# Performance work log

Measured on AMD Instinct MI355X. Metric: run time of the kernel, lower is better.

## Reference

```python
import jax, jax.numpy as jnp
import numpy as np

# Functional model of IntegerLookup.call (CPU DenseHashTable path) applied to a
# fresh table containing only the pre-inserted OOV key (-1 -> 0), i.e. the
# first call after construction. Semantics of that call:
#   - flatten inputs, take unique keys in order of first occurrence
#   - assign contiguous ids starting at table.size()==1, up to max_tokens inserts
#   - keys beyond capacity (and anything not inserted) look up to default 0
# Note: the original code's `vals <= 0` test also re-inserts -1 itself, so -1
# is treated like any other key on the first call; we reproduce that exactly by
# not special-casing -1.

def _integer_lookup(inputs, max_tokens):
    shape = inputs.shape
    x = inputs.reshape(-1)
    n = x.shape[0]
    big = jnp.iinfo(x.dtype).max
    # unique keys (padded to fixed size n) + inverse map element -> unique slot
    uniq, inv = jnp.unique(x, return_inverse=True, size=n, fill_value=big)
    inv = inv.reshape(-1)
    # first-occurrence position of each unique key (padded slots keep sentinel n)
    first_idx = jnp.full((n,), n, dtype=jnp.int32).at[inv].min(
        jnp.arange(n, dtype=jnp.int32))
    # rank uniques by order of first appearance (padded slots sort last)
    rank = jnp.argsort(jnp.argsort(first_idx)).astype(jnp.int32)
    # table starts with size 1 (the -1 -> 0 OOV entry), so ids start at 1;
    # only the first `max_tokens` new keys fit (num_empty_slot), rest -> 0
    id_per_unique = jnp.where(rank < max_tokens, rank + 1, 0).astype(x.dtype)
    return id_per_unique[inv].reshape(shape)


def setup_inputs() -> dict:
    key = jax.random.key(0)
    inputs = jax.random.randint(key, (16384, 200), 0, 2000000, dtype=jnp.int32)
    return {"inputs": inputs, "max_tokens": 1000000}


def reference(inputs, max_tokens):
    return _integer_lookup(inputs, max_tokens)
```

## Files before the change

kernel.cpp:

```cpp
#include <hip/hip_runtime.h>
#include <stdint.h>

#define TABLE_BITS 21
#define TABLE_SIZE (1u << TABLE_BITS)
#define TABLE_MASK (TABLE_SIZE - 1u)
#define BLOCK 256
#define EPT 4
#define CHUNK (BLOCK * EPT)
#define EPT2 16
#define CHUNK2 (BLOCK * EPT2)
#define RANK_BIT 0x40000000
#define RANK_MASK 0x3FFFFFFF
#define NB 256
#define BSHIFT (TABLE_BITS - 8)
#define KPB (1 << BSHIFT)
#define KLOW_MASK (KPB - 1)
#define INF_PAT 0x7f7f7f7f
#define BJ_INVALID 0xFFFFFFFFu

template<int NT>
__device__ __forceinline__ int blk_excl_scan(int v, int tid, int* total) {
    constexpr int NW = NT / 64;
    int lane = tid & 63, w = tid >> 6;
    int inc = v;
    #pragma unroll
    for (int off = 1; off < 64; off <<= 1) {
        int u = __shfl_up(inc, off, 64);
        if (lane >= off) inc += u;
    }
    __shared__ int part[NW];
    if (lane == 63) part[w] = inc;
    __syncthreads();
    if (tid < NW) {
        int p = part[tid];
        #pragma unroll
        for (int off = 1; off < NW; off <<= 1) {
            int u = __shfl_up(p, off, 64);
            if (tid >= off) p += u;
        }
        part[tid] = p;
    }
    __syncthreads();
    int excl = ((w == 0) ? 0 : part[w - 1]) + inc - v;
    int tot = part[NW - 1];
    __syncthreads();
    if (total) *total = tot;
    return excl;
}

__global__ __launch_bounds__(BLOCK) void k_hist(const int* __restrict__ x, int n,
                                                unsigned* __restrict__ hist) {
    __shared__ unsigned cnt[NB];
    int tid = threadIdx.x;
    cnt[tid] = 0;
    __syncthreads();
    int e0 = blockIdx.x * CHUNK2;
    #pragma unroll
    for (int k = 0; k < EPT2 / 4; ++k) {
        int idx = e0 + k * (BLOCK * 4) + tid * 4;
        if (idx + 4 <= n) {
            int4 v = *reinterpret_cast<const int4*>(x + idx);
            atomicAdd(&cnt[((unsigned)v.x & TABLE_MASK) >> BSHIFT], 1u);
            atomicAdd(&cnt[((unsigned)v.y & TABLE_MASK) >> BSHIFT], 1u);
            atomicAdd(&cnt[((unsigned)v.z & TABLE_MASK) >> BSHIFT], 1u);
            atomicAdd(&cnt[((unsigned)v.w & TABLE_MASK) >> BSHIFT], 1u);
        } else {
            for (int i = idx; i < n; ++i)
                atomicAdd(&cnt[((unsigned)x[i] & TABLE_MASK) >> BSHIFT], 1u);
        }
    }
    __syncthreads();
    hist[(size_t)blockIdx.x * NB + tid] = cnt[tid];
}

__global__ __launch_bounds__(256) void k_colscan(unsigned* __restrict__ hist, int SB2,
                                                 unsigned* __restrict__ bucketTot) {
    int j = blockIdx.x, tid = threadIdx.x;
    unsigned carry = 0;
    for (int b0 = 0; b0 < SB2; b0 += 256) {
        int b = b0 + tid;
        int v = (b < SB2) ? (int)hist[(size_t)b * NB + j] : 0;
        int tot;
        int excl = blk_excl_scan<256>(v, tid, &tot);
        if (b < SB2) hist[(size_t)b * NB + j] = carry + (unsigned)excl;
        carry += (unsigned)tot;
    }
    if (tid == 0) bucketTot[j] = carry;
}

__global__ __launch_bounds__(256) void k_bucketbase(const unsigned* __restrict__ bucketTot,
                                                    unsigned* __restrict__ bucketBase) {
    int tid = threadIdx.x;
    int v = (int)bucketTot[tid];
    int tot;
    int excl = blk_excl_scan<256>(v, tid, &tot);
    bucketBase[tid] = (unsigned)excl;
    if (tid == 255) bucketBase[256] = (unsigned)(excl + v);
}

__global__ __launch_bounds__(BLOCK) void k_scatter(const int* __restrict__ x, int n,
                                                   const unsigned* __restrict__ hist,
                                                   const unsigned* __restrict__ bucketBase,
                                                   unsigned long long* __restrict__ pairs) {
    __shared__ unsigned cnt[NB];
    __shared__ unsigned lbase[NB + 1];
    __shared__ unsigned sbase[NB];
    __shared__ unsigned long long lp[CHUNK2];
    int tid = threadIdx.x;
    cnt[tid] = 0;
    sbase[tid] = bucketBase[tid] + hist[(size_t)blockIdx.x * NB + tid];
    __syncthreads();

    unsigned bjs[EPT2], kls[EPT2], los[EPT2];
    int e0 = blockIdx.x * CHUNK2;
    #pragma unroll
    for (int k = 0; k < EPT2 / 4; ++k) {
        int idx = e0 + k * (BLOCK * 4) + tid * 4;
        if (idx + 4 <= n) {
            int4 v = *reinterpret_cast<const int4*>(x + idx);
            unsigned kk[4] = {(unsigned)v.x & TABLE_MASK, (unsigned)v.y & TABLE_MASK,
                              (unsigned)v.z & TABLE_MASK, (unsigned)v.w & TABLE_MASK};
            #pragma unroll
            for (int j = 0; j < 4; ++j) {
                int e = k * 4 + j;
                bjs[e] = kk[j] >> BSHIFT;
                kls[e] = kk[j] & KLOW_MASK;
                los[e] = atomicAdd(&cnt[bjs[e]], 1u);
            }
        } else {
            #pragma unroll
            for (int j = 0; j < 4; ++j) {
                int e = k * 4 + j;
                int i = idx + j;
                if (i < n) {
                    unsigned kv = (unsigned)x[i] & TABLE_MASK;
                    bjs[e] = kv >> BSHIFT;
                    kls[e] = kv & KLOW_MASK;
                    los[e] = atomicAdd(&cnt[bjs[e]], 1u);
                } else {
                    bjs[e] = BJ_INVALID;
                }
            }
        }
    }
    __syncthreads();
    {
        int v = (int)cnt[tid];
        int tot;
        int ex = blk_excl_scan<256>(v, tid, &tot);
        lbase[tid] = (unsigned)ex;
        if (tid == 255) lbase[256] = (unsigned)(ex + v);
    }
    __syncthreads();
    #pragma unroll
    for (int k = 0; k < EPT2 / 4; ++k) {
        #pragma unroll
        for (int j = 0; j < 4; ++j) {
            int e = k * 4 + j;
            if (bjs[e] != BJ_INVALID) {
                unsigned pos = (unsigned)(e0 + k * (BLOCK * 4) + tid * 4 + j);
                lp[lbase[bjs[e]] + los[e]] =
                    ((unsigned long long)kls[e] << 32) | pos;
            }
        }
    }
    __syncthreads();
    int wv = tid >> 6, ln = tid & 63;
    for (int j = wv; j < NB; j += BLOCK / 64) {
        unsigned ls = lbase[j], len = lbase[j + 1] - ls, gs = sbase[j];
        for (unsigned i = ln; i < len; i += 64)
            pairs[gs + i] = lp[ls + i];
    }
}

__global__ __launch_bounds__(512) void k_bucket_min(const unsigned long long* __restrict__ pairs,
                                                    const unsigned* __restrict__ bucketBase,
                                                    int* __restrict__ table,
                                                    unsigned char* __restrict__ flag) {
    __shared__ int fi[KPB];
    int j = blockIdx.x, tid = threadIdx.x;
    for (int k = tid; k < KPB; k += 512) fi[k] = INF_PAT;
    __syncthreads();
    unsigned s = bucketBase[j], e = bucketBase[j + 1];
    for (unsigned idx = s + tid; idx < e; idx += 512) {
        unsigned long long p = pairs[idx];
        atomicMin(&fi[(unsigned)(p >> 32)], (int)(unsigned)p);
    }
    __syncthreads();
    int* dst = table + (size_t)j * KPB;
    for (int k = tid; k < KPB; k += 512) dst[k] = fi[k];
    for (unsigned idx = s + tid; idx < e; idx += 512) {
        unsigned long long p = pairs[idx];
        unsigned pos = (unsigned)p;
        flag[pos] = (unsigned char)(fi[(unsigned)(p >> 32)] == (int)pos);
    }
}

__global__ __launch_bounds__(BLOCK) void k_flags(const unsigned char* __restrict__ flag, int n,
                                                 int* __restrict__ blockSums,
                                                 unsigned long long* __restrict__ bitmask) {
    int tid = threadIdx.x;
    int lane = tid & 63, w = tid >> 6;
    int base = blockIdx.x * CHUNK + tid * EPT;
    int flags[EPT];
    if (base + EPT <= n) {
        uchar4 f = *reinterpret_cast<const uchar4*>(flag + base);
        flags[0] = f.x; flags[1] = f.y; flags[2] = f.z; flags[3] = f.w;
    } else {
        #pragma unroll
        for (int j = 0; j < EPT; ++j)
            flags[j] = (base + j < n) ? flag[base + j] : 0;
    }
    int cnt = 0;
    #pragma unroll
    for (int j = 0; j < EPT; ++j) {
        unsigned long long mj = __ballot(flags[j]);
        if (lane == 0) bitmask[((size_t)blockIdx.x * (BLOCK / 64) + w) * EPT + j] = mj;
        cnt += flags[j];
    }
    for (int off = 32; off > 0; off >>= 1)
        cnt += __shfl_down(cnt, off, 64);
    __shared__ int ws[BLOCK / 64];
    if (lane == 0) ws[w] = cnt;
    __syncthreads();
    if (tid == 0) {
        int s = 0;
        #pragma unroll
        for (int q = 0; q < BLOCK / 64; ++q) s += ws[q];
        blockSums[blockIdx.x] = s;
    }
}

__global__ __launch_bounds__(1024) void k_scan(int* __restrict__ sums, int B) {
    int tid = threadIdx.x;
    int carry = 0;
    for (int b0 = 0; b0 < B; b0 += 1024) {
        int b = b0 + tid;
        int v = (b < B) ? sums[b] : 0;
        int tot;
        int excl = blk_excl_scan<1024>(v, tid, &tot);
        if (b < B) sums[b] = carry + excl;
        carry += tot;
    }
}

__global__ __launch_bounds__(BLOCK) void k_rank(const int* __restrict__ x, int n,
                                                int* __restrict__ table,
                                                const int* __restrict__ blockSums,
                                                const unsigned long long* __restrict__ bitmask) {
    int tid = threadIdx.x;
    int lane = tid & 63, w = tid >> 6;
    int base = blockIdx.x * CHUNK + tid * EPT;
    const unsigned long long* bm = bitmask + ((size_t)blockIdx.x * (BLOCK / 64) + w) * EPT;
    int flags[EPT];
    int cnt = 0;
    #pragma unroll
    for (int j = 0; j < EPT; ++j) {
        flags[j] = (int)((bm[j] >> lane) & 1ull);
        cnt += flags[j];
    }
    __shared__ int lds[BLOCK];
    lds[tid] = cnt;
    __syncthreads();
    for (int off = 1; off < BLOCK; off <<= 1) {
        int t = (tid >= off) ? lds[tid - off] : 0;
        __syncthreads();
        lds[tid] += t;
        __syncthreads();
    }
    int r = blockSums[blockIdx.x] + lds[tid] - cnt;
    if (cnt) {
        if (base + EPT <= n) {
            int4 v = *reinterpret_cast<const int4*>(x + base);
            if (flags[0]) table[(unsigned)v.x & TABLE_MASK] = (r++) | RANK_BIT;
            if (flags[1]) table[(unsigned)v.y & TABLE_MASK] = (r++) | RANK_BIT;
            if (flags[2]) table[(unsigned)v.z & TABLE_MASK] = (r++) | RANK_BIT;
            if (flags[3]) table[(unsigned)v.w & TABLE_MASK] = (r++) | RANK_BIT;
        } else {
            #pragma unroll
            for (int j = 0; j < EPT; ++j)
                if (flags[j]) table[(unsigned)x[base + j] & TABLE_MASK] = (r++) | RANK_BIT;
        }
    }
}

__global__ __launch_bounds__(BLOCK) void k_out(const int* __restrict__ x, int n,
                                               const int* __restrict__ table,
                                               const int* __restrict__ mtp,
                                               int* __restrict__ out) {
    int mt = mtp[0];
    int base = (blockIdx.x * BLOCK + threadIdx.x) * EPT;
    if (base + EPT <= n) {
        int4 v = *reinterpret_cast<const int4*>(x + base);
        int4 o;
        int r;
        r = table[(unsigned)v.x & TABLE_MASK] & RANK_MASK; o.x = (r < mt) ? r + 1 : 0;
        r = table[(unsigned)v.y & TABLE_MASK] & RANK_MASK; o.y = (r < mt) ? r + 1 : 0;
        r = table[(unsigned)v.z & TABLE_MASK] & RANK_MASK; o.z = (r < mt) ? r + 1 : 0;
        r = table[(unsigned)v.w & TABLE_MASK] & RANK_MASK; o.w = (r < mt) ? r + 1 : 0;
        *reinterpret_cast<int4*>(out + base) = o;
    } else {
        for (int i = base; i < n; ++i) {
            int r = table[(unsigned)x[i] & TABLE_MASK] & RANK_MASK;
            out[i] = (r < mt) ? r + 1 : 0;
        }
    }
}

__global__ __launch_bounds__(BLOCK) void k_first_idx(const int* __restrict__ x, int n,
                                                     int* __restrict__ table) {
    int base = (blockIdx.x * BLOCK + threadIdx.x) * EPT;
    for (int i = base; i < min(base + EPT, n); ++i)
        atomicMin(&table[(unsigned)x[i] & TABLE_MASK], i);
}
__global__ __launch_bounds__(BLOCK) void k_count(const int* __restrict__ x, int n,
                                                 const int* __restrict__ table,
                                                 int* __restrict__ blockSums,
                                                 unsigned long long* __restrict__ bitmask) {
    int tid = threadIdx.x;
    int lane = tid & 63, w = tid >> 6;
    int base = blockIdx.x * CHUNK + tid * EPT;
    int flags[EPT];
    #pragma unroll
    for (int j = 0; j < EPT; ++j) {
        flags[j] = 0;
        if (base + j < n)
            flags[j] = (table[(unsigned)x[base + j] & TABLE_MASK] == base + j);
    }
    int cnt = 0;
    #pragma unroll
    for (int j = 0; j < EPT; ++j) {
        unsigned long long mj = __ballot(flags[j]);
        if (lane == 0) bitmask[((size_t)blockIdx.x * (BLOCK / 64) + w) * EPT + j] = mj;
        cnt += flags[j];
    }
    for (int off = 32; off > 0; off >>= 1)
        cnt += __shfl_down(cnt, off, 64);
    __shared__ int ws[BLOCK / 64];
    if (lane == 0) ws[w] = cnt;
    __syncthreads();
    if (tid == 0) {
        int s = 0;
        #pragma unroll
        for (int q = 0; q < BLOCK / 64; ++q) s += ws[q];
        blockSums[blockIdx.x] = s;
    }
}

extern "C" void kernel_launch(void* const* d_in, const int* in_sizes, int n_in,
                              void* d_out, int out_size, void* d_ws, size_t ws_size,
                              hipStream_t stream) {
    const int* x   = (const int*)d_in[0];
    const int* mtp = (const int*)d_in[1];
    int n = in_sizes[0];
    int* out = (int*)d_out;

    int SB  = (n + CHUNK  - 1) / CHUNK;
    int SB2 = (n + CHUNK2 - 1) / CHUNK2;

    auto align16 = [](size_t v) { return (v + 15) & ~(size_t)15; };
    size_t off = 0;
    int* table = (int*)d_ws;                                    off = align16(off + (size_t)TABLE_SIZE * 4);
    unsigned long long* pairs = (unsigned long long*)((char*)d_ws + off); off = align16(off + (size_t)n * 8);
    unsigned char* flag = (unsigned char*)((char*)d_ws + off);  off = align16(off + (size_t)n);
    unsigned* hist = (unsigned*)((char*)d_ws + off);            off = align16(off + (size_t)SB2 * NB * 4);
    unsigned* bucketTot = (unsigned*)((char*)d_ws + off);       off = align16(off + (size_t)NB * 4);
    unsigned* bucketBase = (unsigned*)((char*)d_ws + off);      off = align16(off + (size_t)(NB + 1) * 4);
    int* blockSums = (int*)((char*)d_ws + off);                 off = align16(off + (size_t)SB * 4);
    unsigned long long* bitmask = (unsigned long long*)((char*)d_ws + off);
    off = align16(off + (size_t)SB * (BLOCK / 64) * EPT * 8);

    if (ws_size >= off) {
        k_hist      <<<SB2, BLOCK, 0, stream>>>(x, n, hist);
        k_colscan   <<<NB,  256,   0, stream>>>(hist, SB2, bucketTot);
        k_bucketbase<<<1,   256,   0, stream>>>(bucketTot, bucketBase);
        k_scatter   <<<SB2, BLOCK, 0, stream>>>(x, n, hist, bucketBase, pairs);
        k_bucket_min<<<NB,  512,   0, stream>>>(pairs, bucketBase, table, flag);
        k_flags     <<<SB,  BLOCK, 0, stream>>>(flag, n, blockSums, bitmask);
    } else {
        hipMemsetAsync(table, 0x7F, (size_t)TABLE_SIZE * 4, stream);
        k_first_idx<<<SB, BLOCK, 0, stream>>>(x, n, table);
        k_count    <<<SB, BLOCK, 0, stream>>>(x, n, table, blockSums, bitmask);
    }
    k_scan <<<1, 1024, 0, stream>>>(blockSums, SB);
    k_rank <<<SB, BLOCK, 0, stream>>>(x, n, table, blockSums, bitmask);
    k_out  <<<SB, BLOCK, 0, stream>>>(x, n, table, mtp, out);
}
```

Before: 128.7 us.

## Split key/pos pairs into SoA arrays and compute final ids per bucket

Replaces the 8-byte (key-low, position) pairs with separate 32-bit position and 16-bit key-low arrays, cutting scatter and bucket traffic. Rank assignment moves into a per-bucket kernel that works in LDS, using popcounts over a per-1024-element bitmask. That kernel writes the final clamped id straight into the table slice, so the output kernel becomes a plain gather. k_flags now builds the bitmask with shared atomicOr, and the fallback path gets its own kernels. The cost is a popcount loop of up to 16 words per unique key and a second pass over the bucket arrays.

```diff
diff --git a/kernel.cpp b/kernel.cpp
--- a/kernel.cpp
+++ b/kernel.cpp
@@ -9,14 +9,14 @@
 #define CHUNK (BLOCK * EPT)
 #define EPT2 16
 #define CHUNK2 (BLOCK * EPT2)
-#define RANK_BIT 0x40000000
-#define RANK_MASK 0x3FFFFFFF
 #define NB 256
 #define BSHIFT (TABLE_BITS - 8)
 #define KPB (1 << BSHIFT)
 #define KLOW_MASK (KPB - 1)
 #define INF_PAT 0x7f7f7f7f
 #define BJ_INVALID 0xFFFFFFFFu
+#define RANK_BIT 0x40000000
+#define RANK_MASK 0x3FFFFFFF
 
 template<int NT>
 __device__ __forceinline__ int blk_excl_scan(int v, int tid, int* total) {
@@ -101,11 +101,13 @@
 __global__ __launch_bounds__(BLOCK) void k_scatter(const int* __restrict__ x, int n,
                                                    const unsigned* __restrict__ hist,
                                                    const unsigned* __restrict__ bucketBase,
-                                                   unsigned long long* __restrict__ pairs) {
+                                                   unsigned* __restrict__ posArr,
+                                                   unsigned short* __restrict__ klArr) {
     __shared__ unsigned cnt[NB];
     __shared__ unsigned lbase[NB + 1];
     __shared__ unsigned sbase[NB];
-    __shared__ unsigned long long lp[CHUNK2];
+    __shared__ unsigned lpos[CHUNK2];
+    __shared__ unsigned short lkl[CHUNK2];
     int tid = threadIdx.x;
     cnt[tid] = 0;
     sbase[tid] = bucketBase[tid] + hist[(size_t)blockIdx.x * NB + tid];
@@ -158,9 +160,9 @@
         for (int j = 0; j < 4; ++j) {
             int e = k * 4 + j;
             if (bjs[e] != BJ_INVALID) {
-                unsigned pos = (unsigned)(e0 + k * (BLOCK * 4) + tid * 4 + j);
-                lp[lbase[bjs[e]] + los[e]] =
-                    ((unsigned long long)kls[e] << 32) | pos;
+                unsigned dst = lbase[bjs[e]] + los[e];
+                lpos[dst] = (unsigned)(e0 + k * (BLOCK * 4) + tid * 4 + j);
+                lkl[dst]  = (unsigned short)kls[e];
             }
         }
     }
@@ -168,12 +170,15 @@
     int wv = tid >> 6, ln = tid & 63;
     for (int j = wv; j < NB; j += BLOCK / 64) {
         unsigned ls = lbase[j], len = lbase[j + 1] - ls, gs = sbase[j];
-        for (unsigned i = ln; i < len; i += 64)
-            pairs[gs + i] = lp[ls + i];
-    }
-}
-
-__global__ __launch_bounds__(512) void k_bucket_min(const unsigned long long* __restrict__ pairs,
+        for (unsigned i = ln; i < len; i += 64) {
+            posArr[gs + i] = lpos[ls + i];
+            klArr[gs + i]  = lkl[ls + i];
+        }
+    }
+}
+
+__global__ __launch_bounds__(512) void k_bucket_min(const unsigned* __restrict__ posArr,
+                                                    const unsigned short* __restrict__ klArr,
                                                     const unsigned* __restrict__ bucketBase,
                                                     int* __restrict__ table,
                                                     unsigned char* __restrict__ flag) {
@@ -182,47 +187,44 @@
     for (int k = tid; k < KPB; k += 512) fi[k] = INF_PAT;
     __syncthreads();
     unsigned s = bucketBase[j], e = bucketBase[j + 1];
-    for (unsigned idx = s + tid; idx < e; idx += 512) {
-        unsigned long long p = pairs[idx];
-        atomicMin(&fi[(unsigned)(p >> 32)], (int)(unsigned)p);
-    }
+    for (unsigned idx = s + tid; idx < e; idx += 512)
+        atomicMin(&fi[klArr[idx]], (int)posArr[idx]);
     __syncthreads();
     int* dst = table + (size_t)j * KPB;
     for (int k = tid; k < KPB; k += 512) dst[k] = fi[k];
     for (unsigned idx = s + tid; idx < e; idx += 512) {
-        unsigned long long p = pairs[idx];
-        unsigned pos = (unsigned)p;
-        flag[pos] = (unsigned char)(fi[(unsigned)(p >> 32)] == (int)pos);
+        unsigned pos = posArr[idx];
+        flag[pos] = (unsigned char)(fi[klArr[idx]] == (int)pos);
     }
 }
 
 __global__ __launch_bounds__(BLOCK) void k_flags(const unsigned char* __restrict__ flag, int n,
                                                  int* __restrict__ blockSums,
                                                  unsigned long long* __restrict__ bitmask) {
+    __shared__ unsigned long long words[16];
     int tid = threadIdx.x;
     int lane = tid & 63, w = tid >> 6;
+    if (tid < 16) words[tid] = 0ull;
+    __syncthreads();
     int base = blockIdx.x * CHUNK + tid * EPT;
-    int flags[EPT];
+    unsigned nib = 0;
     if (base + EPT <= n) {
         uchar4 f = *reinterpret_cast<const uchar4*>(flag + base);
-        flags[0] = f.x; flags[1] = f.y; flags[2] = f.z; flags[3] = f.w;
+        nib = (unsigned)f.x | ((unsigned)f.y << 1) | ((unsigned)f.z << 2) | ((unsigned)f.w << 3);
     } else {
         #pragma unroll
         for (int j = 0; j < EPT; ++j)
-            flags[j] = (base + j < n) ? flag[base + j] : 0;
-    }
-    int cnt = 0;
-    #pragma unroll
-    for (int j = 0; j < EPT; ++j) {
-        unsigned long long mj = __ballot(flags[j]);
-        if (lane == 0) bitmask[((size_t)blockIdx.x * (BLOCK / 64) + w) * EPT + j] = mj;
-        cnt += flags[j];
-    }
+            if (base + j < n) nib |= (unsigned)flag[base + j] << j;
+    }
+    if (nib)
+        atomicOr(&words[tid >> 4], (unsigned long long)nib << ((tid * 4) & 63));
+    int cnt = __popc(nib);
     for (int off = 32; off > 0; off >>= 1)
         cnt += __shfl_down(cnt, off, 64);
     __shared__ int ws[BLOCK / 64];
     if (lane == 0) ws[w] = cnt;
     __syncthreads();
+    if (tid < 16) bitmask[(size_t)blockIdx.x * 16 + tid] = words[tid];
     if (tid == 0) {
         int s = 0;
         #pragma unroll
@@ -244,66 +246,54 @@
     }
 }
 
-__global__ __launch_bounds__(BLOCK) void k_rank(const int* __restrict__ x, int n,
-                                                int* __restrict__ table,
-                                                const int* __restrict__ blockSums,
-                                                const unsigned long long* __restrict__ bitmask) {
-    int tid = threadIdx.x;
-    int lane = tid & 63, w = tid >> 6;
-    int base = blockIdx.x * CHUNK + tid * EPT;
-    const unsigned long long* bm = bitmask + ((size_t)blockIdx.x * (BLOCK / 64) + w) * EPT;
-    int flags[EPT];
-    int cnt = 0;
-    #pragma unroll
-    for (int j = 0; j < EPT; ++j) {
-        flags[j] = (int)((bm[j] >> lane) & 1ull);
-        cnt += flags[j];
-    }
-    __shared__ int lds[BLOCK];
-    lds[tid] = cnt;
-    __syncthreads();
-    for (int off = 1; off < BLOCK; off <<= 1) {
-        int t = (tid >= off) ? lds[tid - off] : 0;
-        __syncthreads();
-        lds[tid] += t;
-        __syncthreads();
-    }
-    int r = blockSums[blockIdx.x] + lds[tid] - cnt;
-    if (cnt) {
-        if (base + EPT <= n) {
-            int4 v = *reinterpret_cast<const int4*>(x + base);
-            if (flags[0]) table[(unsigned)v.x & TABLE_MASK] = (r++) | RANK_BIT;
-            if (flags[1]) table[(unsigned)v.y & TABLE_MASK] = (r++) | RANK_BIT;
-            if (flags[2]) table[(unsigned)v.z & TABLE_MASK] = (r++) | RANK_BIT;
-            if (flags[3]) table[(unsigned)v.w & TABLE_MASK] = (r++) | RANK_BIT;
-        } else {
-            #pragma unroll
-            for (int j = 0; j < EPT; ++j)
-                if (flags[j]) table[(unsigned)x[base + j] & TABLE_MASK] = (r++) | RANK_BIT;
-        }
-    }
+__global__ __launch_bounds__(512) void k_rank_bucket(const unsigned* __restrict__ posArr,
+                                                     const unsigned short* __restrict__ klArr,
+                                                     const unsigned* __restrict__ bucketBase,
+                                                     const int* __restrict__ blockSums,
+                                                     const unsigned long long* __restrict__ bitmask,
+                                                     const int* __restrict__ mtp,
+                                                     int* __restrict__ table) {
+    __shared__ int fi[KPB];
+    __shared__ unsigned idv[KPB];
+    int j = blockIdx.x, tid = threadIdx.x;
+    int* slice = table + (size_t)j * KPB;
+    for (int k = tid; k < KPB; k += 512) fi[k] = slice[k];
+    __syncthreads();
+    int mt = mtp[0];
+    unsigned s = bucketBase[j], e = bucketBase[j + 1];
+    for (unsigned idx = s + tid; idx < e; idx += 512) {
+        unsigned pos = posArr[idx];
+        unsigned kl = klArr[idx];
+        if (fi[kl] == (int)pos) {
+            const unsigned long long* bm = bitmask + (size_t)(pos >> 10) * 16;
+            unsigned bit = pos & 1023u;
+            unsigned w0 = bit >> 6, b0 = bit & 63u;
+            int r = blockSums[pos >> 10];
+            for (unsigned w = 0; w < w0; ++w) r += __popcll(bm[w]);
+            r += __popcll(bm[w0] & ((1ull << b0) - 1ull));
+            idv[kl] = (r < mt) ? (unsigned)(r + 1) : 0u;
+        }
+    }
+    __syncthreads();
+    for (int k = tid; k < KPB; k += 512)
+        slice[k] = (fi[k] != INF_PAT) ? (int)idv[k] : 0;
 }
 
 __global__ __launch_bounds__(BLOCK) void k_out(const int* __restrict__ x, int n,
                                                const int* __restrict__ table,
-                                               const int* __restrict__ mtp,
                                                int* __restrict__ out) {
-    int mt = mtp[0];
     int base = (blockIdx.x * BLOCK + threadIdx.x) * EPT;
     if (base + EPT <= n) {
         int4 v = *reinterpret_cast<const int4*>(x + base);
         int4 o;
-        int r;
-        r = table[(unsigned)v.x & TABLE_MASK] & RANK_MASK; o.x = (r < mt) ? r + 1 : 0;
-        r = table[(unsigned)v.y & TABLE_MASK] & RANK_MASK; o.y = (r < mt) ? r + 1 : 0;
-        r = table[(unsigned)v.z & TABLE_MASK] & RANK_MASK; o.z = (r < mt) ? r + 1 : 0;
-        r = table[(unsigned)v.w & TABLE_MASK] & RANK_MASK; o.w = (r < mt) ? r + 1 : 0;
+        o.x = table[(unsigned)v.x & TABLE_MASK];
+        o.y = table[(unsigned)v.y & TABLE_MASK];
+        o.z = table[(unsigned)v.z & TABLE_MASK];
+        o.w = table[(unsigned)v.w & TABLE_MASK];
         *reinterpret_cast<int4*>(out + base) = o;
     } else {
-        for (int i = base; i < n; ++i) {
-            int r = table[(unsigned)x[i] & TABLE_MASK] & RANK_MASK;
-            out[i] = (r < mt) ? r + 1 : 0;
-        }
+        for (int i = base; i < n; ++i)
+            out[i] = table[(unsigned)x[i] & TABLE_MASK];
     }
 }
 
@@ -313,37 +303,49 @@
     for (int i = base; i < min(base + EPT, n); ++i)
         atomicMin(&table[(unsigned)x[i] & TABLE_MASK], i);
 }
-__global__ __launch_bounds__(BLOCK) void k_count(const int* __restrict__ x, int n,
-                                                 const int* __restrict__ table,
-                                                 int* __restrict__ blockSums,
-                                                 unsigned long long* __restrict__ bitmask) {
-    int tid = threadIdx.x;
-    int lane = tid & 63, w = tid >> 6;
+__global__ __launch_bounds__(BLOCK) void k_rank_fb(const int* __restrict__ x, int n,
+                                                   int* __restrict__ table,
+                                                   int* __restrict__ blockSums) {
+    int tid = threadIdx.x;
     int base = blockIdx.x * CHUNK + tid * EPT;
     int flags[EPT];
+    int cnt = 0;
     #pragma unroll
     for (int j = 0; j < EPT; ++j) {
         flags[j] = 0;
         if (base + j < n)
             flags[j] = (table[(unsigned)x[base + j] & TABLE_MASK] == base + j);
-    }
+        cnt += flags[j];
+    }
+    int tot;
+    int r = blockSums[blockIdx.x] + blk_excl_scan<BLOCK>(cnt, tid, &tot);
+    #pragma unroll
+    for (int j = 0; j < EPT; ++j)
+        if (flags[j]) table[(unsigned)x[base + j] & TABLE_MASK] = (r++) | RANK_BIT;
+}
+__global__ __launch_bounds__(BLOCK) void k_count_fb(const int* __restrict__ x, int n,
+                                                    const int* __restrict__ table,
+                                                    int* __restrict__ blockSums) {
+    int tid = threadIdx.x;
+    int base = blockIdx.x * CHUNK + tid * EPT;
     int cnt = 0;
     #pragma unroll
-    for (int j = 0; j < EPT; ++j) {
-        unsigned long long mj = __ballot(flags[j]);
-        if (lane == 0) bitmask[((size_t)blockIdx.x * (BLOCK / 64) + w) * EPT + j] = mj;
-        cnt += flags[j];
-    }
-    for (int off = 32; off > 0; off >>= 1)
-        cnt += __shfl_down(cnt, off, 64);
-    __shared__ int ws[BLOCK / 64];
-    if (lane == 0) ws[w] = cnt;
-    __syncthreads();
-    if (tid == 0) {
-        int s = 0;
-        #pragma unroll
-        for (int q = 0; q < BLOCK / 64; ++q) s += ws[q];
-        blockSums[blockIdx.x] = s;
+    for (int j = 0; j < EPT; ++j)
+        if (base + j < n)
+            cnt += (table[(unsigned)x[base + j] & TABLE_MASK] == base + j);
+    int tot;
+    blk_excl_scan<BLOCK>(cnt, tid, &tot);
+    if (tid == 0) blockSums[blockIdx.x] = tot;
+}
+__global__ __launch_bounds__(BLOCK) void k_out_fb(const int* __restrict__ x, int n,
+                                                  const int* __restrict__ table,
+                                                  const int* __restrict__ mtp,
+                                                  int* __restrict__ out) {
+    int mt = mtp[0];
+    int base = (blockIdx.x * BLOCK + threadIdx.x) * EPT;
+    for (int i = base; i < min(base + EPT, n); ++i) {
+        int r = table[(unsigned)x[i] & TABLE_MASK] & RANK_MASK;
+        out[i] = (r < mt) ? r + 1 : 0;
     }
 }
 
@@ -360,29 +362,36 @@
 
     auto align16 = [](size_t v) { return (v + 15) & ~(size_t)15; };
     size_t off = 0;
-    int* table = (int*)d_ws;                                    off = align16(off + (size_t)TABLE_SIZE * 4);
-    unsigned long long* pairs = (unsigned long long*)((char*)d_ws + off); off = align16(off + (size_t)n * 8);
-    unsigned char* flag = (unsigned char*)((char*)d_ws + off);  off = align16(off + (size_t)n);
-    unsigned* hist = (unsigned*)((char*)d_ws + off);            off = align16(off + (size_t)SB2 * NB * 4);
-    unsigned* bucketTot = (unsigned*)((char*)d_ws + off);       off = align16(off + (size_t)NB * 4);
-    unsigned* bucketBase = (unsigned*)((char*)d_ws + off);      off = align16(off + (size_t)(NB + 1) * 4);
-    int* blockSums = (int*)((char*)d_ws + off);                 off = align16(off + (size_t)SB * 4);
+    int* table = (int*)d_ws;                                      off = align16(off + (size_t)TABLE_SIZE * 4);
+    unsigned* posArr = (unsigned*)((char*)d_ws + off);            off = align16(off + (size_t)n * 4);
+    unsigned short* klArr = (unsigned short*)((char*)d_ws + off); off = align16(off + (size_t)n * 2);
+    unsigned char* flag = (unsigned char*)((char*)d_ws + off);    off = align16(off + (size_t)n);
+    unsigned* hist = (unsigned*)((char*)d_ws + off);              off = align16(off + (size_t)SB2 * NB * 4);
+    unsigned* bucketTot = (unsigned*)((char*)d_ws + off);         off = align16(off + (size_t)NB * 4);
+    unsigned* bucketBase = (unsigned*)((char*)d_ws + off);        off = align16(off + (size_t)(NB + 1) * 4);
+    int* blockSums = (int*)((char*)d_ws + off);                   off = align16(off + (size_t)SB * 4);
     unsigned long long* bitmask = (unsigned long long*)((char*)d_ws + off);
-    off = align16(off + (size_t)SB * (BLOCK / 64) * EPT * 8);
+    off = align16(off + (size_t)SB * 16 * 8);
 
     if (ws_size >= off) {
-        k_hist      <<<SB2, BLOCK, 0, stream>>>(x, n, hist);
-        k_colscan   <<<NB,  256,   0, stream>>>(hist, SB2, bucketTot);
-        k_bucketbase<<<1,   256,   0, stream>>>(bucketTot, bucketBase);
-        k_scatter   <<<SB2, BLOCK, 0, stream>>>(x, n, hist, bucketBase, pairs);
-        k_bucket_min<<<NB,  512,   0, stream>>>(pairs, bucketBase, table, flag);
-        k_flags     <<<SB,  BLOCK, 0, stream>>>(flag, n, blockSums, bitmask);
+        k_hist       <<<SB2, BLOCK, 0, stream>>>(x, n, hist);
+        k_colscan    <<<NB,  256,   0, stream>>>(hist, SB2, bucketTot);
+        k_bucketbase <<<1,   256,   0, stream>>>(bucketTot, bucketBase);
+        k_scatter    <<<SB2, BLOCK, 0, stream>>>(x, n, hist, bucketBase, posArr, klArr);
+        k_bucket_min <<<NB,  512,   0, stream>>>(posArr, klArr, bucketBase, table, flag);
+        k_flags      <<<SB,  BLOCK, 0, stream>>>(flag, n, blockSums, bitmask);
+        k_scan       <<<1,   1024,  0, stream>>>(blockSums, SB);
+        k_rank_bucket<<<NB,  512,   0, stream>>>(posArr, klArr, bucketBase, blockSums,
+                                                 bitmask, mtp, table);
+        k_out        <<<SB,  BLOCK, 0, stream>>>(x, n, table, out);
     } else {
+        size_t foff = align16((size_t)TABLE_SIZE * 4);
+        int* bs = (int*)((char*)d_ws + foff);
         hipMemsetAsync(table, 0x7F, (size_t)TABLE_SIZE * 4, stream);
         k_first_idx<<<SB, BLOCK, 0, stream>>>(x, n, table);
-        k_count    <<<SB, BLOCK, 0, stream>>>(x, n, table, blockSums, bitmask);
-    }
-    k_scan <<<1, 1024, 0, stream>>>(blockSums, SB);
-    k_rank <<<SB, BLOCK, 0, stream>>>(x, n, table, blockSums, bitmask);
-    k_out  <<<SB, BLOCK, 0, stream>>>(x, n, table, mtp, out);
-}
+        k_count_fb <<<SB, BLOCK, 0, stream>>>(x, n, table, bs);
+        k_scan     <<<1, 1024, 0, stream>>>(bs, SB);
+        k_rank_fb  <<<SB, BLOCK, 0, stream>>>(x, n, table, bs);
+        k_out_fb   <<<SB, BLOCK, 0, stream>>>(x, n, table, mtp, out);
+    }
+}
```

Measured after the change: 172.3 us. 33.9% more time.
